# Kernel tuning notes

Measured on AMD Instinct MI355X. Metric: run time of the kernel, lower is better.

The kernel has to match this reference:

```python
import jax, jax.numpy as jnp
import numpy as np

N, E, G = 100000, 600000, 2000
CONV = [128, 256, 256, 256]
LIN = [256, 128, 1]
BN_EPS = 1e-5


def setup_inputs() -> dict:
    key = jax.random.key(0)
    ks = iter(jax.random.split(key, 64))
    inp = {}
    inp["x"] = jax.random.normal(next(ks), (N, CONV[0]), dtype=jnp.float32)
    inp["edge_index"] = jax.random.randint(next(ks), (2, E), 0, N)
    inp["batch"] = jnp.sort(jax.random.randint(next(ks), (N,), 0, G))

    def lin_w(k, i, o):
        return (jax.random.normal(k, (i, o), dtype=jnp.float32) / np.sqrt(i)).astype(jnp.float32)

    # 3 GINConv MLPs: Linear(in,out), BN(out), ReLU, Linear(out,out), ReLU
    for i in range(3):
        ci, co = CONV[i], CONV[i + 1]
        inp[f"c{i}_w1"] = lin_w(next(ks), ci, co)
        inp[f"c{i}_b1"] = jnp.zeros((co,), jnp.float32)
        inp[f"c{i}_g"] = jnp.ones((co,), jnp.float32)
        inp[f"c{i}_be"] = jnp.zeros((co,), jnp.float32)
        inp[f"c{i}_m"] = jax.random.normal(next(ks), (co,), dtype=jnp.float32) * 0.1
        inp[f"c{i}_v"] = jax.random.uniform(next(ks), (co,), minval=0.5, maxval=1.5, dtype=jnp.float32)
        inp[f"c{i}_w2"] = lin_w(next(ks), co, co)
        inp[f"c{i}_b2"] = jnp.zeros((co,), jnp.float32)
    # head: Linear(256,128) + BN(128) + ReLU, Linear(128,1)
    inp["l0_w"] = lin_w(next(ks), LIN[0], LIN[1])
    inp["l0_b"] = jnp.zeros((LIN[1],), jnp.float32)
    inp["l0_g"] = jnp.ones((LIN[1],), jnp.float32)
    inp["l0_be"] = jnp.zeros((LIN[1],), jnp.float32)
    inp["l0_m"] = jax.random.normal(next(ks), (LIN[1],), dtype=jnp.float32) * 0.1
    inp["l0_v"] = jax.random.uniform(next(ks), (LIN[1],), minval=0.5, maxval=1.5, dtype=jnp.float32)
    inp["l1_w"] = lin_w(next(ks), LIN[1], LIN[2])
    inp["l1_b"] = jnp.zeros((LIN[2],), jnp.float32)
    return inp


def _bn(h, g, be, m, v):
    return g * (h - m) * jax.lax.rsqrt(v + BN_EPS) + be


def _gin_conv(x, src, dst, w1, b1, g, be, m, v, w2, b2):
    # GINConv (eps=0): MLP(x + sum_{j in N(i)} x_j); messages x[src] aggregated at dst
    agg = jax.ops.segment_sum(x[src], dst, num_segments=x.shape[0])
    h = (x + agg) @ w1 + b1
    h = jax.nn.relu(_bn(h, g, be, m, v))
    return jax.nn.relu(h @ w2 + b2)


def reference(x, edge_index, batch,
              c0_w1, c0_b1, c0_g, c0_be, c0_m, c0_v, c0_w2, c0_b2,
              c1_w1, c1_b1, c1_g, c1_be, c1_m, c1_v, c1_w2, c1_b2,
              c2_w1, c2_b1, c2_g, c2_be, c2_m, c2_v, c2_w2, c2_b2,
              l0_w, l0_b, l0_g, l0_be, l0_m, l0_v, l1_w, l1_b):
    src, dst = edge_index[0], edge_index[1]
    conv_params = [
        (c0_w1, c0_b1, c0_g, c0_be, c0_m, c0_v, c0_w2, c0_b2),
        (c1_w1, c1_b1, c1_g, c1_be, c1_m, c1_v, c1_w2, c1_b2),
        (c2_w1, c2_b1, c2_g, c2_be, c2_m, c2_v, c2_w2, c2_b2),
    ]
    h = x
    for i, p in enumerate(conv_params):
        h = _gin_conv(h, src, dst, *p)
        if i < 2:
            h = jax.nn.relu(h)  # outer activation (no-op after ReLU, kept for fidelity)
    # global_add_pool over graphs
    h = jax.ops.segment_sum(h, batch, num_segments=G)  # [G, 256]
    h = h @ l0_w + l0_b
    h = _bn(h, l0_g, l0_be, l0_m, l0_v)
    h = jax.nn.relu(h)  # dropout is identity in eval mode
    return h @ l1_w + l1_b  # [G, 1]
```

## Files before the change

kernel.cpp:

```cpp
#include <hip/hip_runtime.h>
#include <hip/hip_bf16.h>

#define BN_EPS 1e-5f

typedef __attribute__((ext_vector_type(8))) short short8;
typedef __attribute__((ext_vector_type(4))) float f32x4;

__device__ __forceinline__ void gll16(const void* g, void* l) {
    __builtin_amdgcn_global_load_lds(
        (const __attribute__((address_space(1))) unsigned int*)g,
        (__attribute__((address_space(3))) unsigned int*)l, 16, 0, 0);
}

__device__ __forceinline__ unsigned pack_bf2(float a, float b) {
    __hip_bfloat16 ba = __float2bfloat16(a);
    __hip_bfloat16 bb = __float2bfloat16(b);
    return (unsigned)(*(unsigned short*)&ba) | ((unsigned)(*(unsigned short*)&bb) << 16);
}

__global__ void hist_kernel(const int* __restrict__ dst, int* __restrict__ off, int E) {
    int e = blockIdx.x * blockDim.x + threadIdx.x;
    if (e < E) atomicAdd(&off[dst[e] + 1], 1);
}

__global__ __launch_bounds__(256) void scan1_kernel(int* __restrict__ data,
                                                    int* __restrict__ sums, int n) {
    __shared__ int sh[256];
    const int t = threadIdx.x;
    const int idx = blockIdx.x * 1024 + t * 4;
    int v[4];
    int s = 0;
#pragma unroll
    for (int j = 0; j < 4; ++j) {
        int x = (idx + j < n) ? data[idx + j] : 0;
        s += x;
        v[j] = s;
    }
    sh[t] = s;
    __syncthreads();
    for (int o = 1; o < 256; o <<= 1) {
        int x = (t >= o) ? sh[t - o] : 0;
        __syncthreads();
        sh[t] += x;
        __syncthreads();
    }
    const int prev = sh[t] - s;
#pragma unroll
    for (int j = 0; j < 4; ++j) {
        if (idx + j < n) data[idx + j] = v[j] + prev;
    }
    if (t == 255) sums[blockIdx.x] = sh[255];
}

__global__ __launch_bounds__(256) void scan2_kernel(int* __restrict__ sums, int nb) {
    __shared__ int sh[256];
    const int t = threadIdx.x;
    sh[t] = (t < nb) ? sums[t] : 0;
    __syncthreads();
    for (int o = 1; o < 256; o <<= 1) {
        int x = (t >= o) ? sh[t - o] : 0;
        __syncthreads();
        sh[t] += x;
        __syncthreads();
    }
    if (t < nb) sums[t] = sh[t];
}

__global__ void scan3_kernel(int* __restrict__ data, const int* __restrict__ sums,
                             int* __restrict__ cursor, int n, int N) {
    int i = blockIdx.x * blockDim.x + threadIdx.x;
    if (i >= n) return;
    int b = i >> 10;
    int v = data[i];
    if (b > 0) { v += sums[b - 1]; data[i] = v; }
    if (i < N) cursor[i] = v;
}

__global__ void fill_kernel(const int* __restrict__ src, const int* __restrict__ dst,
                            int* __restrict__ cursor, int* __restrict__ sorted_src, int E) {
    int e = blockIdx.x * blockDim.x + threadIdx.x;
    if (e >= E) return;
    int p = atomicAdd(&cursor[dst[e]], 1);
    sorted_src[p] = src[e];
}

__global__ void cvt_x_kernel(const float* __restrict__ x, __hip_bfloat16* __restrict__ xb,
                             int N, int total4 ) {
    int i = blockIdx.x * blockDim.x + threadIdx.x;
    if (i >= total4) return;
    int n = i >> 5;
    unsigned lo = 0, hi = 0;
    if (n < N) {
        const float4 v = ((const float4*)x)[i];
        lo = pack_bf2(v.x, v.y);
        hi = pack_bf2(v.z, v.w);
    }
    ((uint2*)xb)[i] = make_uint2(lo, hi);
}

__global__ void wt_all_kernel(const float* __restrict__ w0, const float* __restrict__ w1,
                              const float* __restrict__ w2, const float* __restrict__ w3,
                              const float* __restrict__ w4, const float* __restrict__ w5,
                              __hip_bfloat16* __restrict__ o0, __hip_bfloat16* __restrict__ o1,
                              __hip_bfloat16* __restrict__ o2, __hip_bfloat16* __restrict__ o3,
                              __hip_bfloat16* __restrict__ o4, __hip_bfloat16* __restrict__ o5) {
    int i = blockIdx.x * blockDim.x + threadIdx.x;
    const int S0 = 256 * 128, S = 256 * 256;
    if (i < S0) {
        int m = i / 128, k = i - m * 128;
        o0[i] = __float2bfloat16(w0[k * 256 + m]);
        return;
    }
    i -= S0;
    int mi = i / S, j = i - mi * S;
    if (mi >= 5) return;
    int m = j >> 8, k = j & 255;
    const float* Wp; __hip_bfloat16* Op;
    switch (mi) {
        case 0: Wp = w1; Op = o1; break;
        case 1: Wp = w2; Op = o2; break;
        case 2: Wp = w3; Op = o3; break;
        case 3: Wp = w4; Op = o4; break;
        default: Wp = w5; Op = o5; break;
    }
    Op[j] = __float2bfloat16(Wp[k * 256 + m]);
}

__global__ void prep_ss_kernel(
    const float* __restrict__ g0, const float* __restrict__ be0, const float* __restrict__ m0,
    const float* __restrict__ v0, const float* __restrict__ b10, const float* __restrict__ b20,
    const float* __restrict__ g1, const float* __restrict__ be1, const float* __restrict__ m1,
    const float* __restrict__ v1, const float* __restrict__ b11, const float* __restrict__ b21,
    const float* __restrict__ g2, const float* __restrict__ be2, const float* __restrict__ m2,
    const float* __restrict__ v2, const float* __restrict__ b12, const float* __restrict__ b22,
    float* __restrict__ ss) {
    const int layer = blockIdx.x;
    const int c = threadIdx.x;
    const float *g, *be, *m, *v, *b1, *b2;
    switch (layer) {
        case 0: g = g0; be = be0; m = m0; v = v0; b1 = b10; b2 = b20; break;
        case 1: g = g1; be = be1; m = m1; v = v1; b1 = b11; b2 = b21; break;
        default: g = g2; be = be2; m = m2; v = v2; b1 = b12; b2 = b22; break;
    }
    float r = rsqrtf(v[c] + BN_EPS);
    float s = g[c] * r;
    ss[(2 * layer) * 512 + c] = s;
    ss[(2 * layer) * 512 + 256 + c] = (b1[c] - m[c]) * s + be[c];
    ss[(2 * layer + 1) * 512 + c] = 1.f;
    ss[(2 * layer + 1) * 512 + 256 + c] = b2[c];
}

template <int C>
__global__ __launch_bounds__(256) void agg_fused(const __hip_bfloat16* __restrict__ h,
                                                 const int* __restrict__ off,
                                                 const int* __restrict__ ssrc,
                                                 __hip_bfloat16* __restrict__ out, int N) {
    constexpr int L = C / 8;
    int t = blockIdx.x * blockDim.x + threadIdx.x;
    int n = t / L;
    if (n >= N) return;
    int c8 = t - n * L;
    const uint4* hp = (const uint4*)h;

    float acc[8];
    {
        uint4 sv = hp[(size_t)n * L + c8];
        const unsigned u[4] = {sv.x, sv.y, sv.z, sv.w};
#pragma unroll
        for (int j = 0; j < 4; ++j) {
            acc[2 * j]     = __uint_as_float(u[j] << 16);
            acc[2 * j + 1] = __uint_as_float(u[j] & 0xffff0000u);
        }
    }
    const int e0 = off[n], e1 = off[n + 1];
    int e = e0;
    for (; e + 2 <= e1; e += 2) {
        int s0 = ssrc[e], s1 = ssrc[e + 1];
        uint4 a = hp[(size_t)s0 * L + c8];
        uint4 b = hp[(size_t)s1 * L + c8];
        const unsigned ua[4] = {a.x, a.y, a.z, a.w};
        const unsigned ub[4] = {b.x, b.y, b.z, b.w};
#pragma unroll
        for (int j = 0; j < 4; ++j) {
            acc[2 * j]     += __uint_as_float(ua[j] << 16);
            acc[2 * j + 1] += __uint_as_float(ua[j] & 0xffff0000u);
            acc[2 * j]     += __uint_as_float(ub[j] << 16);
            acc[2 * j + 1] += __uint_as_float(ub[j] & 0xffff0000u);
        }
    }
    if (e < e1) {
        int s0 = ssrc[e];
        uint4 a = hp[(size_t)s0 * L + c8];
        const unsigned ua[4] = {a.x, a.y, a.z, a.w};
#pragma unroll
        for (int j = 0; j < 4; ++j) {
            acc[2 * j]     += __uint_as_float(ua[j] << 16);
            acc[2 * j + 1] += __uint_as_float(ua[j] & 0xffff0000u);
        }
    }
    unsigned o[4];
#pragma unroll
    for (int j = 0; j < 4; ++j) o[j] = pack_bf2(acc[2 * j], acc[2 * j + 1]);
    ((uint4*)out)[(size_t)n * L + c8] = make_uint4(o[0], o[1], o[2], o[3]);
}

template <int K1>
__global__ __launch_bounds__(512, 4) void mlp_fused(
    const __hip_bfloat16* __restrict__ A,
    const __hip_bfloat16* __restrict__ W1t,
    const __hip_bfloat16* __restrict__ W2t,
    const float* __restrict__ ss1, const float* __restrict__ ss2,
    __hip_bfloat16* __restrict__ C) {
    __shared__ __align__(16) char bufT[32 * 1024];

    const int tid = threadIdx.x;
    const int l   = tid & 63;
    const int w   = tid >> 6;
    const int l15 = l & 15;
    const int kg  = l >> 4;
    const size_t row0 = (size_t)blockIdx.x * 64;

    constexpr int ROWB = K1 * 2;
    constexpr int NT1  = K1 / 32;

    short8 wr1[2][NT1];
    {
        const char* Wb = (const char*)W1t + (size_t)(w * 32 + l15) * ROWB + kg * 16;
#pragma unroll
        for (int i = 0; i < 2; ++i)
#pragma unroll
            for (int t = 0; t < NT1; ++t)
                wr1[i][t] = *(const short8*)(Wb + (size_t)i * 16 * ROWB + t * 64);
    }

    {
        const char* Ab = (const char*)(A + row0 * K1);
#pragma unroll
        for (int ib = w; ib < 4 * NT1; ib += 8) {
            const int j = ib / NT1, t = ib % NT1;
            gll16(Ab + (size_t)(j * 16 + l15) * ROWB + t * 64 + kg * 16,
                  bufT + ib * 1024);
        }
    }
    asm volatile("s_waitcnt vmcnt(0)" ::: "memory");
    __syncthreads();

    f32x4 acc[2][4] = {};
#pragma unroll
    for (int t = 0; t < NT1; ++t) {
        short8 af[4];
#pragma unroll
        for (int j = 0; j < 4; ++j)
            af[j] = *(const short8*)(bufT + (j * NT1 + t) * 1024 + l * 16);
#pragma unroll
        for (int j = 0; j < 4; ++j) {
            acc[0][j] = __builtin_amdgcn_mfma_f32_16x16x32_bf16(wr1[0][t], af[j], acc[0][j], 0, 0, 0);
            acc[1][j] = __builtin_amdgcn_mfma_f32_16x16x32_bf16(wr1[1][t], af[j], acc[1][j], 0, 0, 0);
        }
    }
    __syncthreads();

    short8 wr2[2][8];
    {
        const char* Wb = (const char*)W2t + (size_t)(w * 32 + l15) * 512 + kg * 16;
#pragma unroll
        for (int i = 0; i < 2; ++i)
#pragma unroll
            for (int t = 0; t < 8; ++t)
                wr2[i][t] = *(const short8*)(Wb + (size_t)i * 16 * 512 + t * 64);
    }

#pragma unroll
    for (int i = 0; i < 2; ++i) {
        const int m0 = w * 32 + i * 16 + kg * 4;
        const float4 s4 = *(const float4*)(ss1 + m0);
        const float4 h4 = *(const float4*)(ss1 + 256 + m0);
        const int toff = w * 1024 + (i * 2 + (kg >> 1)) * 256 + l15 * 16 + (kg & 1) * 8;
#pragma unroll
        for (int j = 0; j < 4; ++j) {
            const float v0 = fmaxf(acc[i][j][0] * s4.x + h4.x, 0.f);
            const float v1 = fmaxf(acc[i][j][1] * s4.y + h4.y, 0.f);
            const float v2 = fmaxf(acc[i][j][2] * s4.z + h4.z, 0.f);
            const float v3 = fmaxf(acc[i][j][3] * s4.w + h4.w, 0.f);
            *(uint2*)(bufT + j * 8192 + toff) = make_uint2(pack_bf2(v0, v1), pack_bf2(v2, v3));
        }
    }
    __syncthreads();

    f32x4 acc2[2][4] = {};
#pragma unroll
    for (int t = 0; t < 8; ++t) {
        short8 tf[4];
#pragma unroll
        for (int j = 0; j < 4; ++j)
            tf[j] = *(const short8*)(bufT + (j * 8 + t) * 1024 + l * 16);
#pragma unroll
        for (int j = 0; j < 4; ++j) {
            acc2[0][j] = __builtin_amdgcn_mfma_f32_16x16x32_bf16(wr2[0][t], tf[j], acc2[0][j], 0, 0, 0);
            acc2[1][j] = __builtin_amdgcn_mfma_f32_16x16x32_bf16(wr2[1][t], tf[j], acc2[1][j], 0, 0, 0);
        }
    }
    __syncthreads();

#pragma unroll
    for (int i = 0; i < 2; ++i) {
        const int c0 = w * 32 + i * 16 + kg * 4;
        const float4 s4 = *(const float4*)(ss2 + c0);
        const float4 h4 = *(const float4*)(ss2 + 256 + c0);
        const int toff = w * 1024 + (i * 2 + (kg >> 1)) * 256 + l15 * 16 + (kg & 1) * 8;
#pragma unroll
        for (int j = 0; j < 4; ++j) {
            const float v0 = fmaxf(acc2[i][j][0] * s4.x + h4.x, 0.f);
            const float v1 = fmaxf(acc2[i][j][1] * s4.y + h4.y, 0.f);
            const float v2 = fmaxf(acc2[i][j][2] * s4.z + h4.z, 0.f);
            const float v3 = fmaxf(acc2[i][j][3] * s4.w + h4.w, 0.f);
            *(uint2*)(bufT + j * 8192 + toff) = make_uint2(pack_bf2(v0, v1), pack_bf2(v2, v3));
        }
    }
    __syncthreads();

    {
        char* Cb = (char*)C + row0 * 512;
#pragma unroll
        for (int q = tid; q < 2048; q += 512) {
            const int j  = q >> 9;
            const int wp = (q >> 6) & 7;
            const int lp = q & 63;
            uint4 v = *(const uint4*)(bufT + q * 16);
            *(uint4*)(Cb + (size_t)(j * 16 + (lp & 15)) * 512 + wp * 64 + (lp >> 4) * 16) = v;
        }
    }
}

__device__ __forceinline__ int lower_bound_dev(const int* __restrict__ a, int n, int key) {
    int lo = 0, hi = n;
    while (lo < hi) {
        int mid = (lo + hi) >> 1;
        if (a[mid] < key) lo = mid + 1; else hi = mid;
    }
    return lo;
}

__global__ __launch_bounds__(256) void pool_seg_kernel(const __hip_bfloat16* __restrict__ h,
                                                       const int* __restrict__ batch,
                                                       float* __restrict__ pooled, int N) {
    __shared__ int seg[2];
    const int g = blockIdx.x;
    if (threadIdx.x == 0) seg[0] = lower_bound_dev(batch, N, g);
    if (threadIdx.x == 1) seg[1] = lower_bound_dev(batch, N, g + 1);
    __syncthreads();
    const int c = threadIdx.x;
    float acc = 0.f;
    for (int n = seg[0]; n < seg[1]; ++n) acc += __bfloat162float(h[(size_t)n * 256 + c]);
    pooled[(size_t)g * 256 + c] = acc;
}

__global__ __launch_bounds__(128) void head_kernel(
    const float* __restrict__ pooled,
    const float* __restrict__ w0, const float* __restrict__ b0,
    const float* __restrict__ g, const float* __restrict__ be,
    const float* __restrict__ m, const float* __restrict__ v,
    const float* __restrict__ w1, const float* __restrict__ b1,
    float* __restrict__ out) {
    __shared__ float row[256];
    __shared__ float red[128];
    const int gid = blockIdx.x;
    const int j = threadIdx.x;

    row[j]       = pooled[(size_t)gid * 256 + j];
    row[j + 128] = pooled[(size_t)gid * 256 + 128 + j];
    __syncthreads();

    float acc = b0[j];
#pragma unroll 8
    for (int k = 0; k < 256; ++k) acc += row[k] * w0[k * 128 + j];

    float h = g[j] * (acc - m[j]) * rsqrtf(v[j] + BN_EPS) + be[j];
    h = fmaxf(h, 0.f) * w1[j];
    red[j] = h;
    __syncthreads();
    for (int s = 64; s > 0; s >>= 1) {
        if (j < s) red[j] += red[j + s];
        __syncthreads();
    }
    if (j == 0) out[gid] = red[0] + b1[0];
}

extern "C" void kernel_launch(void* const* d_in, const int* in_sizes, int n_in,
                              void* d_out, int out_size, void* d_ws, size_t ws_size,
                              hipStream_t stream) {
    const float* x    = (const float*)d_in[0];
    const int* eidx   = (const int*)d_in[1];
    const int* batch  = (const int*)d_in[2];

    const int N = in_sizes[0] / 128;
    const int E = in_sizes[1] / 2;
    const int G = out_size;

    const int* src = eidx;
    const int* dst = eidx + E;

    const float* cw1[3]; const float* cb1[3]; const float* cg[3]; const float* cbe[3];
    const float* cm[3];  const float* cv[3];  const float* cw2[3]; const float* cb2[3];
    for (int i = 0; i < 3; ++i) {
        int b = 3 + i * 8;
        cw1[i] = (const float*)d_in[b + 0];
        cb1[i] = (const float*)d_in[b + 1];
        cg[i]  = (const float*)d_in[b + 2];
        cbe[i] = (const float*)d_in[b + 3];
        cm[i]  = (const float*)d_in[b + 4];
        cv[i]  = (const float*)d_in[b + 5];
        cw2[i] = (const float*)d_in[b + 6];
        cb2[i] = (const float*)d_in[b + 7];
    }
    const float* l0_w  = (const float*)d_in[27];
    const float* l0_b  = (const float*)d_in[28];
    const float* l0_g  = (const float*)d_in[29];
    const float* l0_be = (const float*)d_in[30];
    const float* l0_m  = (const float*)d_in[31];
    const float* l0_v  = (const float*)d_in[32];
    const float* l1_w  = (const float*)d_in[33];
    const float* l1_b  = (const float*)d_in[34];

    float* outp = (float*)d_out;

    const int nrb  = (N + 127) / 128;
    const int Npad = nrb * 128;
    const int nrb64 = Npad / 64;
    const size_t SB = (size_t)Npad * 256 * 2;
    const size_t XB = (size_t)Npad * 128 * 2;
    const size_t PB = (size_t)G * 256 * 4;
    const size_t WTB = (size_t)256 * 256 * 2;

    char* ws = (char*)d_ws;
    size_t o = 0;
    __hip_bfloat16* U  = (__hip_bfloat16*)(ws + o); o += SB;
    __hip_bfloat16* V  = (__hip_bfloat16*)(ws + o); o += SB;
    __hip_bfloat16* xb = (__hip_bfloat16*)(ws + o); o += XB;
    float* pooled      = (float*)(ws + o);       o += PB;
    __hip_bfloat16* wt[6];
    for (int i = 0; i < 6; ++i) { wt[i] = (__hip_bfloat16*)(ws + o); o += WTB; }
    float* ss          = (float*)(ws + o);       o += 6 * 512 * 4;
    int* csr_off    = (int*)(ws + o); o += (size_t)(N + 1) * 4;
    int* cursor     = (int*)(ws + o); o += (size_t)N * 4;
    int* sorted_src = (int*)(ws + o); o += (size_t)E * 4;
    int* sums       = (int*)(ws + o); o += 256 * 4;
    if (ws_size < o) return;

    const dim3 blk(256);

    {
        int total4 = Npad * 128 / 4;
        cvt_x_kernel<<<(total4 + 255) / 256, blk, 0, stream>>>(x, xb, N, total4);
    }
    {
        int total = 256 * 128 + 5 * 256 * 256;
        wt_all_kernel<<<(total + 255) / 256, blk, 0, stream>>>(
            cw1[0], cw2[0], cw1[1], cw2[1], cw1[2], cw2[2],
            wt[0], wt[1], wt[2], wt[3], wt[4], wt[5]);
    }
    prep_ss_kernel<<<3, blk, 0, stream>>>(
        cg[0], cbe[0], cm[0], cv[0], cb1[0], cb2[0],
        cg[1], cbe[1], cm[1], cv[1], cb1[1], cb2[1],
        cg[2], cbe[2], cm[2], cv[2], cb1[2], cb2[2], ss);

    {
        const int n_off = N + 1;
        hipMemsetAsync(csr_off, 0, (size_t)n_off * sizeof(int), stream);
        hist_kernel<<<(E + 255) / 256, blk, 0, stream>>>(dst, csr_off, E);
        const int nb = (n_off + 1023) / 1024;
        scan1_kernel<<<nb, blk, 0, stream>>>(csr_off, sums, n_off);
        scan2_kernel<<<1, blk, 0, stream>>>(sums, nb);
        scan3_kernel<<<(n_off + 255) / 256, blk, 0, stream>>>(csr_off, sums, cursor, n_off, N);
        fill_kernel<<<(E + 255) / 256, blk, 0, stream>>>(src, dst, cursor, sorted_src, E);
    }

    auto SS = [&](int i) { return ss + i * 512; };

    {
        int total = N * 16;
        agg_fused<128><<<(total + 255) / 256, blk, 0, stream>>>(xb, csr_off, sorted_src, U, N);
    }
    mlp_fused<128><<<nrb64, dim3(512), 0, stream>>>(U, wt[0], wt[1], SS(0), SS(1), V);

    {
        int total = N * 32;
        agg_fused<256><<<(total + 255) / 256, blk, 0, stream>>>(V, csr_off, sorted_src, U, N);
    }
    mlp_fused<256><<<nrb64, dim3(512), 0, stream>>>(U, wt[2], wt[3], SS(2), SS(3), U);

    {
        int total = N * 32;
        agg_fused<256><<<(total + 255) / 256, blk, 0, stream>>>(U, csr_off, sorted_src, V, N);
    }
    mlp_fused<256><<<nrb64, dim3(512), 0, stream>>>(V, wt[4], wt[5], SS(4), SS(5), V);

    pool_seg_kernel<<<G, blk, 0, stream>>>(V, batch, pooled, N);
    head_kernel<<<G, dim3(128), 0, stream>>>(pooled, l0_w, l0_b, l0_g, l0_be, l0_m, l0_v,
                                             l1_w, l1_b, outp);
}
```

Baseline: 464.0 us.

## Double MLP row tile to 128 and stream weight fragments instead of preloading

Result: faster. 410.5 us (-11.5%).

```diff
diff --git a/kernel.cpp b/kernel.cpp
--- a/kernel.cpp
+++ b/kernel.cpp
@@ -211,32 +211,28 @@
     const __hip_bfloat16* __restrict__ W2t,
     const float* __restrict__ ss1, const float* __restrict__ ss2,
     __hip_bfloat16* __restrict__ C) {
-    __shared__ __align__(16) char bufT[32 * 1024];
+    __shared__ __align__(16) char bufT[64 * 1024];
 
     const int tid = threadIdx.x;
     const int l   = tid & 63;
     const int w   = tid >> 6;
     const int l15 = l & 15;
     const int kg  = l >> 4;
-    const size_t row0 = (size_t)blockIdx.x * 64;
+    const size_t row0 = (size_t)blockIdx.x * 128;
 
     constexpr int ROWB = K1 * 2;
     constexpr int NT1  = K1 / 32;
 
-    short8 wr1[2][NT1];
-    {
-        const char* Wb = (const char*)W1t + (size_t)(w * 32 + l15) * ROWB + kg * 16;
-#pragma unroll
-        for (int i = 0; i < 2; ++i)
-#pragma unroll
-            for (int t = 0; t < NT1; ++t)
-                wr1[i][t] = *(const short8*)(Wb + (size_t)i * 16 * ROWB + t * 64);
-    }
+    const char* W1base = (const char*)W1t + (size_t)(w * 32 + l15) * ROWB + kg * 16;
+    const char* W2base = (const char*)W2t + (size_t)(w * 32 + l15) * 512 + kg * 16;
+
+    short8 wc0 = *(const short8*)(W1base);
+    short8 wc1 = *(const short8*)(W1base + 16 * ROWB);
 
     {
         const char* Ab = (const char*)(A + row0 * K1);
 #pragma unroll
-        for (int ib = w; ib < 4 * NT1; ib += 8) {
+        for (int ib = w; ib < 8 * NT1; ib += 8) {
             const int j = ib / NT1, t = ib % NT1;
             gll16(Ab + (size_t)(j * 16 + l15) * ROWB + t * 64 + kg * 16,
                   bufT + ib * 1024);
@@ -245,30 +241,37 @@
     asm volatile("s_waitcnt vmcnt(0)" ::: "memory");
     __syncthreads();
 
-    f32x4 acc[2][4] = {};
-#pragma unroll
-    for (int t = 0; t < NT1; ++t) {
-        short8 af[4];
-#pragma unroll
-        for (int j = 0; j < 4; ++j)
-            af[j] = *(const short8*)(bufT + (j * NT1 + t) * 1024 + l * 16);
-#pragma unroll
-        for (int j = 0; j < 4; ++j) {
-            acc[0][j] = __builtin_amdgcn_mfma_f32_16x16x32_bf16(wr1[0][t], af[j], acc[0][j], 0, 0, 0);
-            acc[1][j] = __builtin_amdgcn_mfma_f32_16x16x32_bf16(wr1[1][t], af[j], acc[1][j], 0, 0, 0);
-        }
-    }
-    __syncthreads();
-
-    short8 wr2[2][8];
-    {
-        const char* Wb = (const char*)W2t + (size_t)(w * 32 + l15) * 512 + kg * 16;
-#pragma unroll
-        for (int i = 0; i < 2; ++i)
-#pragma unroll
-            for (int t = 0; t < 8; ++t)
-                wr2[i][t] = *(const short8*)(Wb + (size_t)i * 16 * 512 + t * 64);
-    }
+    f32x4 acc1[2][8] = {};
+    {
+        auto step = [&](int t, short8 wa, short8 wb) {
+#pragma unroll
+            for (int jh = 0; jh < 2; ++jh) {
+                short8 af[4];
+#pragma unroll
+                for (int jj = 0; jj < 4; ++jj)
+                    af[jj] = *(const short8*)(bufT + ((jh * 4 + jj) * NT1 + t) * 1024 + l * 16);
+#pragma unroll
+                for (int jj = 0; jj < 4; ++jj) {
+                    acc1[0][jh * 4 + jj] = __builtin_amdgcn_mfma_f32_16x16x32_bf16(
+                        wa, af[jj], acc1[0][jh * 4 + jj], 0, 0, 0);
+                    acc1[1][jh * 4 + jj] = __builtin_amdgcn_mfma_f32_16x16x32_bf16(
+                        wb, af[jj], acc1[1][jh * 4 + jj], 0, 0, 0);
+                }
+            }
+        };
+#pragma unroll 1
+        for (int t = 0; t < NT1 - 1; ++t) {
+            short8 wn0 = *(const short8*)(W1base + (t + 1) * 64);
+            short8 wn1 = *(const short8*)(W1base + 16 * ROWB + (t + 1) * 64);
+            step(t, wc0, wc1);
+            wc0 = wn0; wc1 = wn1;
+        }
+        step(NT1 - 1, wc0, wc1);
+    }
+    __syncthreads();
+
+    wc0 = *(const short8*)(W2base);
+    wc1 = *(const short8*)(W2base + 16 * 512);
 
 #pragma unroll
     for (int i = 0; i < 2; ++i) {
@@ -277,28 +280,42 @@
         const float4 h4 = *(const float4*)(ss1 + 256 + m0);
         const int toff = w * 1024 + (i * 2 + (kg >> 1)) * 256 + l15 * 16 + (kg & 1) * 8;
 #pragma unroll
-        for (int j = 0; j < 4; ++j) {
-            const float v0 = fmaxf(acc[i][j][0] * s4.x + h4.x, 0.f);
-            const float v1 = fmaxf(acc[i][j][1] * s4.y + h4.y, 0.f);
-            const float v2 = fmaxf(acc[i][j][2] * s4.z + h4.z, 0.f);
-            const float v3 = fmaxf(acc[i][j][3] * s4.w + h4.w, 0.f);
+        for (int j = 0; j < 8; ++j) {
+            const float v0 = fmaxf(acc1[i][j][0] * s4.x + h4.x, 0.f);
+            const float v1 = fmaxf(acc1[i][j][1] * s4.y + h4.y, 0.f);
+            const float v2 = fmaxf(acc1[i][j][2] * s4.z + h4.z, 0.f);
+            const float v3 = fmaxf(acc1[i][j][3] * s4.w + h4.w, 0.f);
             *(uint2*)(bufT + j * 8192 + toff) = make_uint2(pack_bf2(v0, v1), pack_bf2(v2, v3));
         }
     }
     __syncthreads();
 
-    f32x4 acc2[2][4] = {};
-#pragma unroll
-    for (int t = 0; t < 8; ++t) {
-        short8 tf[4];
-#pragma unroll
-        for (int j = 0; j < 4; ++j)
-            tf[j] = *(const short8*)(bufT + (j * 8 + t) * 1024 + l * 16);
-#pragma unroll
-        for (int j = 0; j < 4; ++j) {
-            acc2[0][j] = __builtin_amdgcn_mfma_f32_16x16x32_bf16(wr2[0][t], tf[j], acc2[0][j], 0, 0, 0);
-            acc2[1][j] = __builtin_amdgcn_mfma_f32_16x16x32_bf16(wr2[1][t], tf[j], acc2[1][j], 0, 0, 0);
-        }
+    f32x4 acc2[2][8] = {};
+    {
+        auto step = [&](int t, short8 wa, short8 wb) {
+#pragma unroll
+            for (int jh = 0; jh < 2; ++jh) {
+                short8 tf[4];
+#pragma unroll
+                for (int jj = 0; jj < 4; ++jj)
+                    tf[jj] = *(const short8*)(bufT + ((jh * 4 + jj) * 8 + t) * 1024 + l * 16);
+#pragma unroll
+                for (int jj = 0; jj < 4; ++jj) {
+                    acc2[0][jh * 4 + jj] = __builtin_amdgcn_mfma_f32_16x16x32_bf16(
+                        wa, tf[jj], acc2[0][jh * 4 + jj], 0, 0, 0);
+                    acc2[1][jh * 4 + jj] = __builtin_amdgcn_mfma_f32_16x16x32_bf16(
+                        wb, tf[jj], acc2[1][jh * 4 + jj], 0, 0, 0);
+                }
+            }
+        };
+#pragma unroll 1
+        for (int t = 0; t < 7; ++t) {
+            short8 wn0 = *(const short8*)(W2base + (t + 1) * 64);
+            short8 wn1 = *(const short8*)(W2base + 16 * 512 + (t + 1) * 64);
+            step(t, wc0, wc1);
+            wc0 = wn0; wc1 = wn1;
+        }
+        step(7, wc0, wc1);
     }
     __syncthreads();
 
@@ -309,7 +326,7 @@
         const float4 h4 = *(const float4*)(ss2 + 256 + c0);
         const int toff = w * 1024 + (i * 2 + (kg >> 1)) * 256 + l15 * 16 + (kg & 1) * 8;
 #pragma unroll
-        for (int j = 0; j < 4; ++j) {
+        for (int j = 0; j < 8; ++j) {
             const float v0 = fmaxf(acc2[i][j][0] * s4.x + h4.x, 0.f);
             const float v1 = fmaxf(acc2[i][j][1] * s4.y + h4.y, 0.f);
             const float v2 = fmaxf(acc2[i][j][2] * s4.z + h4.z, 0.f);
@@ -322,7 +339,7 @@
     {
         char* Cb = (char*)C + row0 * 512;
 #pragma unroll
-        for (int q = tid; q < 2048; q += 512) {
+        for (int q = tid; q < 4096; q += 512) {
             const int j  = q >> 9;
             const int wp = (q >> 6) & 7;
             const int lp = q & 63;
@@ -426,7 +443,6 @@
 
     const int nrb  = (N + 127) / 128;
     const int Npad = nrb * 128;
-    const int nrb64 = Npad / 64;
     const size_t SB = (size_t)Npad * 256 * 2;
     const size_t XB = (size_t)Npad * 128 * 2;
     const size_t PB = (size_t)G * 256 * 4;
@@ -481,19 +497,19 @@
         int total = N * 16;
         agg_fused<128><<<(total + 255) / 256, blk, 0, stream>>>(xb, csr_off, sorted_src, U, N);
     }
-    mlp_fused<128><<<nrb64, dim3(512), 0, stream>>>(U, wt[0], wt[1], SS(0), SS(1), V);
+    mlp_fused<128><<<nrb, dim3(512), 0, stream>>>(U, wt[0], wt[1], SS(0), SS(1), V);
 
     {
         int total = N * 32;
         agg_fused<256><<<(total + 255) / 256, blk, 0, stream>>>(V, csr_off, sorted_src, U, N);
     }
-    mlp_fused<256><<<nrb64, dim3(512), 0, stream>>>(U, wt[2], wt[3], SS(2), SS(3), U);
+    mlp_fused<256><<<nrb, dim3(512), 0, stream>>>(U, wt[2], wt[3], SS(2), SS(3), U);
 
     {
         int total = N * 32;
         agg_fused<256><<<(total + 255) / 256, blk, 0, stream>>>(U, csr_off, sorted_src, V, N);
     }
-    mlp_fused<256><<<nrb64, dim3(512), 0, stream>>>(V, wt[4], wt[5], SS(4), SS(5), V);
+    mlp_fused<256><<<nrb, dim3(512), 0, stream>>>(V, wt[4], wt[5], SS(4), SS(5), V);
 
     pool_seg_kernel<<<G, blk, 0, stream>>>(V, batch, pooled, N);
     head_kernel<<<G, dim3(128), 0, stream>>>(pooled, l0_w, l0_b, l0_g, l0_be, l0_m, l0_v,
```

## Use 4-wave MLP blocks with 64-column tiles and streamed weight fragments

Applied to the files above, without the earlier changes.

After: 479.0 us. 1.03x slower.

```diff
diff --git a/kernel.cpp b/kernel.cpp
--- a/kernel.cpp
+++ b/kernel.cpp
@@ -205,7 +205,7 @@
 }
 
 template <int K1>
-__global__ __launch_bounds__(512, 4) void mlp_fused(
+__global__ __launch_bounds__(256, 3) void mlp_fused(
     const __hip_bfloat16* __restrict__ A,
     const __hip_bfloat16* __restrict__ W1t,
     const __hip_bfloat16* __restrict__ W2t,
@@ -223,20 +223,29 @@
     constexpr int ROWB = K1 * 2;
     constexpr int NT1  = K1 / 32;
 
-    short8 wr1[2][NT1];
-    {
-        const char* Wb = (const char*)W1t + (size_t)(w * 32 + l15) * ROWB + kg * 16;
-#pragma unroll
-        for (int i = 0; i < 2; ++i)
-#pragma unroll
-            for (int t = 0; t < NT1; ++t)
-                wr1[i][t] = *(const short8*)(Wb + (size_t)i * 16 * ROWB + t * 64);
-    }
+    const char* W1base = (const char*)W1t + (size_t)(w * 64 + l15) * ROWB + kg * 16;
+    const char* W2base = (const char*)W2t + (size_t)(w * 64 + l15) * 512 + kg * 16;
+
+    auto loadW1 = [&](short8* d, int t) {
+#pragma unroll
+        for (int ii = 0; ii < 4; ++ii)
+            d[ii] = *(const short8*)(W1base + (size_t)ii * 16 * ROWB + t * 64);
+    };
+    auto loadW2 = [&](short8* d, int t) {
+#pragma unroll
+        for (int ii = 0; ii < 4; ++ii)
+            d[ii] = *(const short8*)(W2base + (size_t)ii * 16 * 512 + t * 64);
+    };
+
+    short8 wpa[4], wpb[4], wpc[4], wpd[4];
+
+    loadW1(wpa, 0); loadW1(wpb, 1);
+    if (NT1 > 2) { loadW1(wpc, 2); loadW1(wpd, 3); }
 
     {
         const char* Ab = (const char*)(A + row0 * K1);
 #pragma unroll
-        for (int ib = w; ib < 4 * NT1; ib += 8) {
+        for (int ib = w; ib < 4 * NT1; ib += 4) {
             const int j = ib / NT1, t = ib % NT1;
             gll16(Ab + (size_t)(j * 16 + l15) * ROWB + t * 64 + kg * 16,
                   bufT + ib * 1024);
@@ -245,76 +254,88 @@
     asm volatile("s_waitcnt vmcnt(0)" ::: "memory");
     __syncthreads();
 
-    f32x4 acc[2][4] = {};
-#pragma unroll
-    for (int t = 0; t < NT1; ++t) {
-        short8 af[4];
-#pragma unroll
-        for (int j = 0; j < 4; ++j)
-            af[j] = *(const short8*)(bufT + (j * NT1 + t) * 1024 + l * 16);
-#pragma unroll
-        for (int j = 0; j < 4; ++j) {
-            acc[0][j] = __builtin_amdgcn_mfma_f32_16x16x32_bf16(wr1[0][t], af[j], acc[0][j], 0, 0, 0);
-            acc[1][j] = __builtin_amdgcn_mfma_f32_16x16x32_bf16(wr1[1][t], af[j], acc[1][j], 0, 0, 0);
-        }
-    }
-    __syncthreads();
-
-    short8 wr2[2][8];
-    {
-        const char* Wb = (const char*)W2t + (size_t)(w * 32 + l15) * 512 + kg * 16;
-#pragma unroll
-        for (int i = 0; i < 2; ++i)
-#pragma unroll
-            for (int t = 0; t < 8; ++t)
-                wr2[i][t] = *(const short8*)(Wb + (size_t)i * 16 * 512 + t * 64);
-    }
-
-#pragma unroll
-    for (int i = 0; i < 2; ++i) {
-        const int m0 = w * 32 + i * 16 + kg * 4;
+    f32x4 acc1[4][4] = {};
+    {
+        auto step = [&](int t, const short8* wf) {
+            short8 af[4];
+#pragma unroll
+            for (int jj = 0; jj < 4; ++jj)
+                af[jj] = *(const short8*)(bufT + (size_t)(jj * NT1 + t) * 1024 + l * 16);
+#pragma unroll
+            for (int ii = 0; ii < 4; ++ii)
+#pragma unroll
+                for (int jj = 0; jj < 4; ++jj)
+                    acc1[ii][jj] = __builtin_amdgcn_mfma_f32_16x16x32_bf16(
+                        wf[ii], af[jj], acc1[ii][jj], 0, 0, 0);
+        };
+#pragma unroll 1
+        for (int t = 0; t < NT1; t += 4) {
+            step(t + 0, wpa); if (t + 4 < NT1) loadW1(wpa, t + 4);
+            step(t + 1, wpb); if (t + 5 < NT1) loadW1(wpb, t + 5);
+            step(t + 2, wpc); if (t + 6 < NT1) loadW1(wpc, t + 6);
+            step(t + 3, wpd); if (t + 7 < NT1) loadW1(wpd, t + 7);
+        }
+    }
+    __syncthreads();
+
+    loadW2(wpa, 0); loadW2(wpb, 1); loadW2(wpc, 2); loadW2(wpd, 3);
+
+#pragma unroll
+    for (int ii = 0; ii < 4; ++ii) {
+        const int m0 = w * 64 + ii * 16 + kg * 4;
         const float4 s4 = *(const float4*)(ss1 + m0);
         const float4 h4 = *(const float4*)(ss1 + 256 + m0);
-        const int toff = w * 1024 + (i * 2 + (kg >> 1)) * 256 + l15 * 16 + (kg & 1) * 8;
-#pragma unroll
-        for (int j = 0; j < 4; ++j) {
-            const float v0 = fmaxf(acc[i][j][0] * s4.x + h4.x, 0.f);
-            const float v1 = fmaxf(acc[i][j][1] * s4.y + h4.y, 0.f);
-            const float v2 = fmaxf(acc[i][j][2] * s4.z + h4.z, 0.f);
-            const float v3 = fmaxf(acc[i][j][3] * s4.w + h4.w, 0.f);
-            *(uint2*)(bufT + j * 8192 + toff) = make_uint2(pack_bf2(v0, v1), pack_bf2(v2, v3));
-        }
-    }
-    __syncthreads();
-
-    f32x4 acc2[2][4] = {};
-#pragma unroll
-    for (int t = 0; t < 8; ++t) {
-        short8 tf[4];
-#pragma unroll
-        for (int j = 0; j < 4; ++j)
-            tf[j] = *(const short8*)(bufT + (j * 8 + t) * 1024 + l * 16);
-#pragma unroll
-        for (int j = 0; j < 4; ++j) {
-            acc2[0][j] = __builtin_amdgcn_mfma_f32_16x16x32_bf16(wr2[0][t], tf[j], acc2[0][j], 0, 0, 0);
-            acc2[1][j] = __builtin_amdgcn_mfma_f32_16x16x32_bf16(wr2[1][t], tf[j], acc2[1][j], 0, 0, 0);
-        }
-    }
-    __syncthreads();
-
-#pragma unroll
-    for (int i = 0; i < 2; ++i) {
-        const int c0 = w * 32 + i * 16 + kg * 4;
+        const int toff = (w * 2 + (ii >> 1)) * 1024 +
+                         (((ii & 1) << 1) | (kg >> 1)) * 256 + l15 * 16 + (kg & 1) * 8;
+#pragma unroll
+        for (int jj = 0; jj < 4; ++jj) {
+            const float v0 = fmaxf(acc1[ii][jj][0] * s4.x + h4.x, 0.f);
+            const float v1 = fmaxf(acc1[ii][jj][1] * s4.y + h4.y, 0.f);
+            const float v2 = fmaxf(acc1[ii][jj][2] * s4.z + h4.z, 0.f);
+            const float v3 = fmaxf(acc1[ii][jj][3] * s4.w + h4.w, 0.f);
+            *(uint2*)(bufT + jj * 8192 + toff) = make_uint2(pack_bf2(v0, v1), pack_bf2(v2, v3));
+        }
+    }
+    __syncthreads();
+
+    f32x4 acc2[4][4] = {};
+    {
+        auto step = [&](int t, const short8* wf) {
+            short8 tf[4];
+#pragma unroll
+            for (int jj = 0; jj < 4; ++jj)
+                tf[jj] = *(const short8*)(bufT + (size_t)(jj * 8 + t) * 1024 + l * 16);
+#pragma unroll
+            for (int ii = 0; ii < 4; ++ii)
+#pragma unroll
+                for (int jj = 0; jj < 4; ++jj)
+                    acc2[ii][jj] = __builtin_amdgcn_mfma_f32_16x16x32_bf16(
+                        wf[ii], tf[jj], acc2[ii][jj], 0, 0, 0);
+        };
+#pragma unroll 1
+        for (int t = 0; t < 8; t += 4) {
+            step(t + 0, wpa); if (t + 4 < 8) loadW2(wpa, t + 4);
+            step(t + 1, wpb); if (t + 5 < 8) loadW2(wpb, t + 5);
+            step(t + 2, wpc); if (t + 6 < 8) loadW2(wpc, t + 6);
+            step(t + 3, wpd); if (t + 7 < 8) loadW2(wpd, t + 7);
+        }
+    }
+    __syncthreads();
+
+#pragma unroll
+    for (int ii = 0; ii < 4; ++ii) {
+        const int c0 = w * 64 + ii * 16 + kg * 4;
         const float4 s4 = *(const float4*)(ss2 + c0);
         const float4 h4 = *(const float4*)(ss2 + 256 + c0);
-        const int toff = w * 1024 + (i * 2 + (kg >> 1)) * 256 + l15 * 16 + (kg & 1) * 8;
-#pragma unroll
-        for (int j = 0; j < 4; ++j) {
-            const float v0 = fmaxf(acc2[i][j][0] * s4.x + h4.x, 0.f);
-            const float v1 = fmaxf(acc2[i][j][1] * s4.y + h4.y, 0.f);
-            const float v2 = fmaxf(acc2[i][j][2] * s4.z + h4.z, 0.f);
-            const float v3 = fmaxf(acc2[i][j][3] * s4.w + h4.w, 0.f);
-            *(uint2*)(bufT + j * 8192 + toff) = make_uint2(pack_bf2(v0, v1), pack_bf2(v2, v3));
+        const int toff = (w * 2 + (ii >> 1)) * 1024 +
+                         (((ii & 1) << 1) | (kg >> 1)) * 256 + l15 * 16 + (kg & 1) * 8;
+#pragma unroll
+        for (int jj = 0; jj < 4; ++jj) {
+            const float v0 = fmaxf(acc2[ii][jj][0] * s4.x + h4.x, 0.f);
+            const float v1 = fmaxf(acc2[ii][jj][1] * s4.y + h4.y, 0.f);
+            const float v2 = fmaxf(acc2[ii][jj][2] * s4.z + h4.z, 0.f);
+            const float v3 = fmaxf(acc2[ii][jj][3] * s4.w + h4.w, 0.f);
+            *(uint2*)(bufT + jj * 8192 + toff) = make_uint2(pack_bf2(v0, v1), pack_bf2(v2, v3));
         }
     }
     __syncthreads();
@@ -322,12 +343,13 @@
     {
         char* Cb = (char*)C + row0 * 512;
 #pragma unroll
-        for (int q = tid; q < 2048; q += 512) {
-            const int j  = q >> 9;
-            const int wp = (q >> 6) & 7;
-            const int lp = q & 63;
+        for (int q = tid; q < 2048; q += 256) {
+            const int ib  = q >> 6;
+            const int j   = ib >> 3;
+            const int t2  = ib & 7;
+            const int lid = q & 63;
             uint4 v = *(const uint4*)(bufT + q * 16);
-            *(uint4*)(Cb + (size_t)(j * 16 + (lp & 15)) * 512 + wp * 64 + (lp >> 4) * 16) = v;
+            *(uint4*)(Cb + (size_t)(j * 16 + (lid & 15)) * 512 + t2 * 64 + (lid >> 4) * 16) = v;
         }
     }
 }
@@ -481,19 +503,19 @@
         int total = N * 16;
         agg_fused<128><<<(total + 255) / 256, blk, 0, stream>>>(xb, csr_off, sorted_src, U, N);
     }
-    mlp_fused<128><<<nrb64, dim3(512), 0, stream>>>(U, wt[0], wt[1], SS(0), SS(1), V);
+    mlp_fused<128><<<nrb64, blk, 0, stream>>>(U, wt[0], wt[1], SS(0), SS(1), V);
 
     {
         int total = N * 32;
         agg_fused<256><<<(total + 255) / 256, blk, 0, stream>>>(V, csr_off, sorted_src, U, N);
     }
-    mlp_fused<256><<<nrb64, dim3(512), 0, stream>>>(U, wt[2], wt[3], SS(2), SS(3), U);
+    mlp_fused<256><<<nrb64, blk, 0, stream>>>(U, wt[2], wt[3], SS(2), SS(3), U);
 
     {
         int total = N * 32;
         agg_fused<256><<<(total + 255) / 256, blk, 0, stream>>>(U, csr_off, sorted_src, V, N);
     }
-    mlp_fused<256><<<nrb64, dim3(512), 0, stream>>>(V, wt[4], wt[5], SS(4), SS(5), V);
+    mlp_fused<256><<<nrb64, blk, 0, stream>>>(V, wt[4], wt[5], SS(4), SS(5), V);
 
     pool_seg_kernel<<<G, blk, 0, stream>>>(V, batch, pooled, N);
     head_kernel<<<G, dim3(128), 0, stream>>>(pooled, l0_w, l0_b, l0_g, l0_be, l0_m, l0_v,
```
